# Optimization experiments

Hardware: AMD Instinct MI355X
Metric: run time of the kernel (lower is better)

Reference implementation:

```python
import jax, jax.numpy as jnp
import numpy as np

TOP_K = 2

def setup_inputs() -> dict:
    key = jax.random.key(0)
    k1, k2, k3, k4, k5 = jax.random.split(key, 5)
    B, S, H, E, F = 2, 1024, 1024, 8, 2816
    scale = 0.02
    return {
        "hidden_states": jax.random.normal(k1, (B, S, H), dtype=jnp.float32),
        "gate_w": jax.random.normal(k2, (E, H), dtype=jnp.float32) * scale,
        "w1": jax.random.normal(k3, (E, H, F), dtype=jnp.float32) * scale,
        "w3": jax.random.normal(k4, (E, H, F), dtype=jnp.float32) * scale,
        "w2": jax.random.normal(k5, (E, F, H), dtype=jnp.float32) * scale,
    }

def reference(hidden_states, gate_w, w1, w3, w2):
    B, S, H = hidden_states.shape
    E = gate_w.shape[0]
    x = hidden_states.reshape(-1, H)                      # [T, H]
    T = x.shape[0]
    # Router: logits -> fp32 softmax -> top-k -> renormalize
    router_logits = jnp.einsum('th,eh->te', x, gate_w)    # [T, E]
    probs = jax.nn.softmax(router_logits.astype(jnp.float32), axis=-1)
    top_w, top_i = jax.lax.top_k(probs, TOP_K)            # [T, k]
    top_w = top_w / jnp.sum(top_w, axis=-1, keepdims=True)
    # Scatter normalized top-k weights into dense combine matrix [T, E]
    combine = jnp.zeros((T, E), dtype=probs.dtype)
    combine = combine.at[jnp.arange(T)[:, None], top_i].set(top_w)
    combine = combine.astype(x.dtype)
    # Experts: SwiGLU MLP per expert, weighted combine (dense formulation
    # of gather -> grouped GEMM -> scatter; non-selected experts get weight 0)
    g = jnp.einsum('th,ehf->tef', x, w1)                  # gate proj
    u = jnp.einsum('th,ehf->tef', x, w3)                  # up proj
    act = jax.nn.silu(g) * u                              # [T, E, F]
    act = act * combine[:, :, None]                       # apply routing weight
    out = jnp.einsum('tef,efh->th', act, w2)              # down proj + combine
    final_hidden_states = out.reshape(B, S, H)
    return final_hidden_states, router_logits
```

## Files before the change

### kernel.cpp

```cpp
#include <hip/hip_runtime.h>

typedef unsigned short u16;
typedef unsigned int u32;
typedef __attribute__((ext_vector_type(8))) short bf16x8;
typedef __attribute__((ext_vector_type(4))) float f32x4;

#define T_TOK 2048
#define H_DIM 1024
#define E_NUM 8
#define F_DIM 2816
#define BM 64
#define BN 64
#define BK 32

__device__ __forceinline__ u16 f2bf(float f) {
    u32 b = __float_as_uint(f);
    u32 lsb = (b >> 16) & 1u;
    b += 0x7fffu + lsb;
    return (u16)(b >> 16);
}

__global__ __launch_bounds__(64) void router_kernel(
    const float* __restrict__ x, const float* __restrict__ gw,
    float* __restrict__ logits_out, int* __restrict__ cnt,
    int* __restrict__ tok_list, float* __restrict__ wt_list)
{
    int t = blockIdx.x;
    int lane = threadIdx.x;
    const float* xr = x + (size_t)t * H_DIM;

    float acc[E_NUM];
#pragma unroll
    for (int e = 0; e < E_NUM; e++) acc[e] = 0.f;

    for (int j = 0; j < H_DIM / 64; j++) {
        int idx = j * 64 + lane;
        float xv = xr[idx];
#pragma unroll
        for (int e = 0; e < E_NUM; e++)
            acc[e] += xv * gw[e * H_DIM + idx];
    }
#pragma unroll
    for (int e = 0; e < E_NUM; e++) {
        float v = acc[e];
#pragma unroll
        for (int o = 32; o > 0; o >>= 1) v += __shfl_xor(v, o, 64);
        acc[e] = v;
    }
    if (lane == 0) {
#pragma unroll
        for (int e = 0; e < E_NUM; e++) logits_out[t * E_NUM + e] = acc[e];
        float m = acc[0];
#pragma unroll
        for (int e = 1; e < E_NUM; e++) m = fmaxf(m, acc[e]);
        float p[E_NUM], s = 0.f;
#pragma unroll
        for (int e = 0; e < E_NUM; e++) { p[e] = expf(acc[e] - m); s += p[e]; }
        float inv = 1.f / s;
#pragma unroll
        for (int e = 0; e < E_NUM; e++) p[e] *= inv;
        int i0 = 0;
#pragma unroll
        for (int e = 1; e < E_NUM; e++) if (p[e] > p[i0]) i0 = e;
        int i1 = (i0 == 0) ? 1 : 0;
#pragma unroll
        for (int e = 0; e < E_NUM; e++) if (e != i0 && p[e] > p[i1]) i1 = e;
        float w0 = p[i0], w1 = p[i1];
        float rs = 1.f / (w0 + w1);
        w0 *= rs; w1 *= rs;
        int s0 = atomicAdd(&cnt[i0], 1);
        tok_list[i0 * T_TOK + s0] = t; wt_list[i0 * T_TOK + s0] = w0;
        int s1 = atomicAdd(&cnt[i1], 1);
        tok_list[i1 * T_TOK + s1] = t; wt_list[i1 * T_TOK + s1] = w1;
    }
}

__global__ void offsets_kernel(const int* __restrict__ cnt, int* __restrict__ off)
{
    if (threadIdx.x == 0 && blockIdx.x == 0) {
        int s = 0;
        for (int e = 0; e < E_NUM; e++) {
            off[e] = s;
            s += ((cnt[e] + BM - 1) / BM) * BM;
        }
    }
}

__global__ __launch_bounds__(256) void gemm1_kernel(
    const float* __restrict__ x, const float* __restrict__ w1,
    const float* __restrict__ w3, const int* __restrict__ cnt,
    const int* __restrict__ off, const int* __restrict__ tok_list,
    const float* __restrict__ wt_list, u16* __restrict__ act)
{
    int e = blockIdx.z;
    int m0 = blockIdx.y * BM;
    int n0 = blockIdx.x * BN;
    int c = cnt[e];
    if (m0 >= c) return;

    __shared__ __align__(16) u16 As[BM][40];
    __shared__ __align__(16) u16 B1[BN][40];
    __shared__ __align__(16) u16 B3[BN][40];
    __shared__ int tok_s[BM];
    __shared__ float wt_s[BM];

    int tid = threadIdx.x;
    if (tid < BM) {
        int tok = tok_list[e * T_TOK + m0 + tid];
        tok_s[tid] = tok;
        wt_s[tid] = (tok >= 0) ? wt_list[e * T_TOK + m0 + tid] : 0.f;
    }
    __syncthreads();

    int w = tid >> 6, lane = tid & 63, q = lane >> 4, l15 = lane & 15;
    int wm = (w >> 1) * 32, wn = (w & 1) * 32;

    f32x4 zero = {0.f, 0.f, 0.f, 0.f};
    f32x4 accg[2][2], accu[2][2];
#pragma unroll
    for (int tm = 0; tm < 2; tm++)
#pragma unroll
        for (int tn = 0; tn < 2; tn++) { accg[tm][tn] = zero; accu[tm][tn] = zero; }

    int ar = tid >> 2, ac0 = (tid & 3) * 8;
    int bk = tid >> 3, bf0 = (tid & 7) * 8;
    int tokA = tok_s[ar];
    const size_t wbase = (size_t)e * H_DIM * F_DIM;

    for (int k0 = 0; k0 < H_DIM; k0 += BK) {
        float a8[8];
#pragma unroll
        for (int i = 0; i < 8; i++) a8[i] = 0.f;
        if (tokA >= 0) {
            float4 v0 = *(const float4*)(x + (size_t)tokA * H_DIM + k0 + ac0);
            float4 v1 = *(const float4*)(x + (size_t)tokA * H_DIM + k0 + ac0 + 4);
            a8[0] = v0.x; a8[1] = v0.y; a8[2] = v0.z; a8[3] = v0.w;
            a8[4] = v1.x; a8[5] = v1.y; a8[6] = v1.z; a8[7] = v1.w;
        }
        union { uint4 v; u16 u[8]; } au;
#pragma unroll
        for (int i = 0; i < 8; i++) au.u[i] = f2bf(a8[i]);
        *(uint4*)&As[ar][ac0] = au.v;

        const size_t boff = wbase + (size_t)(k0 + bk) * F_DIM + n0 + bf0;
        float4 b1a = *(const float4*)(w1 + boff);
        float4 b1b = *(const float4*)(w1 + boff + 4);
        float4 b3a = *(const float4*)(w3 + boff);
        float4 b3b = *(const float4*)(w3 + boff + 4);
        float b1v[8] = {b1a.x, b1a.y, b1a.z, b1a.w, b1b.x, b1b.y, b1b.z, b1b.w};
        float b3v[8] = {b3a.x, b3a.y, b3a.z, b3a.w, b3b.x, b3b.y, b3b.z, b3b.w};
#pragma unroll
        for (int i = 0; i < 8; i++) {
            B1[bf0 + i][bk] = f2bf(b1v[i]);
            B3[bf0 + i][bk] = f2bf(b3v[i]);
        }
        __syncthreads();

        bf16x8 a[2], b1f[2], b3f[2];
#pragma unroll
        for (int tm = 0; tm < 2; tm++)
            a[tm] = *(const bf16x8*)&As[wm + tm * 16 + l15][q * 8];
#pragma unroll
        for (int tn = 0; tn < 2; tn++) {
            b1f[tn] = *(const bf16x8*)&B1[wn + tn * 16 + l15][q * 8];
            b3f[tn] = *(const bf16x8*)&B3[wn + tn * 16 + l15][q * 8];
        }
#pragma unroll
        for (int tm = 0; tm < 2; tm++)
#pragma unroll
            for (int tn = 0; tn < 2; tn++) {
                accg[tm][tn] = __builtin_amdgcn_mfma_f32_16x16x32_bf16(a[tm], b1f[tn], accg[tm][tn], 0, 0, 0);
                accu[tm][tn] = __builtin_amdgcn_mfma_f32_16x16x32_bf16(a[tm], b3f[tn], accu[tm][tn], 0, 0, 0);
            }
        __syncthreads();
    }

    int pos0 = off[e] + m0;
#pragma unroll
    for (int tm = 0; tm < 2; tm++)
#pragma unroll
        for (int tn = 0; tn < 2; tn++)
#pragma unroll
            for (int r = 0; r < 4; r++) {
                int row = wm + tm * 16 + q * 4 + r;
                float g = accg[tm][tn][r];
                float u = accu[tm][tn][r];
                float wt = wt_s[row];
                float sg = g / (1.f + expf(-g));
                float val = sg * u * wt;
                int col = n0 + wn + tn * 16 + l15;
                act[(size_t)(pos0 + row) * F_DIM + col] = f2bf(val);
            }
}

__global__ __launch_bounds__(256) void gemm2_kernel(
    const u16* __restrict__ act, const float* __restrict__ w2,
    const int* __restrict__ cnt, const int* __restrict__ off,
    const int* __restrict__ tok_list, float* __restrict__ accum)
{
    int e = blockIdx.z;
    int m0 = blockIdx.y * BM;
    int n0 = blockIdx.x * BN;
    int c = cnt[e];
    if (m0 >= c) return;

    __shared__ __align__(16) u16 As[BM][40];
    __shared__ __align__(16) u16 Bt[BN][40];
    __shared__ int tok_s[BM];

    int tid = threadIdx.x;
    if (tid < BM) tok_s[tid] = tok_list[e * T_TOK + m0 + tid];
    __syncthreads();

    int w = tid >> 6, lane = tid & 63, q = lane >> 4, l15 = lane & 15;
    int wm = (w >> 1) * 32, wn = (w & 1) * 32;

    f32x4 zero = {0.f, 0.f, 0.f, 0.f};
    f32x4 acc[2][2];
#pragma unroll
    for (int tm = 0; tm < 2; tm++)
#pragma unroll
        for (int tn = 0; tn < 2; tn++) acc[tm][tn] = zero;

    int ar = tid >> 2, ac0 = (tid & 3) * 8;
    int bk = tid >> 3, bf0 = (tid & 7) * 8;
    const size_t arow = (size_t)(off[e] + m0 + ar) * F_DIM;
    const size_t wbase = (size_t)e * F_DIM * H_DIM;

    for (int k0 = 0; k0 < F_DIM; k0 += BK) {
        uint4 av = *(const uint4*)(act + arow + k0 + ac0);
        *(uint4*)&As[ar][ac0] = av;

        const size_t boff = wbase + (size_t)(k0 + bk) * H_DIM + n0 + bf0;
        float4 ba = *(const float4*)(w2 + boff);
        float4 bb = *(const float4*)(w2 + boff + 4);
        float bv[8] = {ba.x, ba.y, ba.z, ba.w, bb.x, bb.y, bb.z, bb.w};
#pragma unroll
        for (int i = 0; i < 8; i++) Bt[bf0 + i][bk] = f2bf(bv[i]);
        __syncthreads();

        bf16x8 a[2], b[2];
#pragma unroll
        for (int tm = 0; tm < 2; tm++)
            a[tm] = *(const bf16x8*)&As[wm + tm * 16 + l15][q * 8];
#pragma unroll
        for (int tn = 0; tn < 2; tn++)
            b[tn] = *(const bf16x8*)&Bt[wn + tn * 16 + l15][q * 8];
#pragma unroll
        for (int tm = 0; tm < 2; tm++)
#pragma unroll
            for (int tn = 0; tn < 2; tn++)
                acc[tm][tn] = __builtin_amdgcn_mfma_f32_16x16x32_bf16(a[tm], b[tn], acc[tm][tn], 0, 0, 0);
        __syncthreads();
    }

#pragma unroll
    for (int tm = 0; tm < 2; tm++)
#pragma unroll
        for (int tn = 0; tn < 2; tn++)
#pragma unroll
            for (int r = 0; r < 4; r++) {
                int row = wm + tm * 16 + q * 4 + r;
                int tok = tok_s[row];
                if (tok >= 0) {
                    int col = n0 + wn + tn * 16 + l15;
                    atomicAdd(&accum[(size_t)tok * H_DIM + col], acc[tm][tn][r]);
                }
            }
}

__global__ __launch_bounds__(256) void conv_kernel(
    const float* __restrict__ accum, float* __restrict__ out)
{
    int i = blockIdx.x * 256 + threadIdx.x;
    out[i] = accum[i];
}

extern "C" void kernel_launch(void* const* d_in, const int* in_sizes, int n_in,
                              void* d_out, int out_size, void* d_ws, size_t ws_size,
                              hipStream_t stream) {
    const float* x  = (const float*)d_in[0];
    const float* gw = (const float*)d_in[1];
    const float* w1 = (const float*)d_in[2];
    const float* w3 = (const float*)d_in[3];
    const float* w2 = (const float*)d_in[4];
    float* out = (float*)d_out;

    char* ws = (char*)d_ws;
    int*   cnt      = (int*)(ws);
    int*   off      = (int*)(ws + 64);
    int*   tok_list = (int*)(ws + 128);
    float* wt_list  = (float*)(ws + 128 + 65536);
    float* accum    = (float*)(ws + 128 + 131072);
    u16*   act      = (u16*)(ws + 128 + 131072 + 8388608);

    hipMemsetAsync(cnt, 0, 64, stream);
    hipMemsetAsync(tok_list, 0xFF, 65536, stream);
    hipMemsetAsync(accum, 0, (size_t)T_TOK * H_DIM * 4, stream);

    float* logits_out = out + (size_t)T_TOK * H_DIM;
    router_kernel<<<T_TOK, 64, 0, stream>>>(x, gw, logits_out, cnt, tok_list, wt_list);
    offsets_kernel<<<1, 64, 0, stream>>>(cnt, off);
    gemm1_kernel<<<dim3(F_DIM / BN, T_TOK / BM, E_NUM), 256, 0, stream>>>(
        x, w1, w3, cnt, off, tok_list, wt_list, act);
    gemm2_kernel<<<dim3(H_DIM / BN, T_TOK / BM, E_NUM), 256, 0, stream>>>(
        act, w2, cnt, off, tok_list, accum);
    conv_kernel<<<(T_TOK * H_DIM) / 256, 256, 0, stream>>>(accum, out);
}
```

Measured before the change: 695.7 us.

## Enlarge MoE GEMM tiles, coalesce weight loads, and drop accumulate-copy kernel

Grows the gate/up GEMM tile to 128x128 and the down GEMM tile to 128x64, so each wave computes a 64x64 or 64x32 sub-tile with more MFMAs per shared-memory fetch. Weight tiles are now read with each thread walking down a column, so neighbouring threads read neighbouring addresses, and each thread writes one vectorized shared-memory store instead of eight scalar transposed stores. Global loads are issued before the barrier that guards the shared-memory overwrite, which lets the next tile's loads overlap the current compute and removes the trailing barrier. The down projection now adds atomically straight into the output, so the separate fp32 accumulator and the copy kernel are dropped. The costs are higher register pressure, fewer blocks for small per-expert counts, and more row padding per expert.

New measurement: 667.1 us. 4.1% less time.

```diff
diff --git a/kernel.cpp b/kernel.cpp
--- a/kernel.cpp
+++ b/kernel.cpp
@@ -9,9 +9,11 @@
 #define H_DIM 1024
 #define E_NUM 8
 #define F_DIM 2816
-#define BM 64
-#define BN 64
+#define BM 128
+#define BN1 128
+#define BN2 64
 #define BK 32
+#define LDK 40
 
 __device__ __forceinline__ u16 f2bf(float f) {
     u32 b = __float_as_uint(f);
@@ -86,7 +88,7 @@
     }
 }
 
-__global__ __launch_bounds__(256) void gemm1_kernel(
+__global__ __launch_bounds__(256, 2) void gemm1_kernel(
     const float* __restrict__ x, const float* __restrict__ w1,
     const float* __restrict__ w3, const int* __restrict__ cnt,
     const int* __restrict__ off, const int* __restrict__ tok_list,
@@ -94,13 +96,12 @@
 {
     int e = blockIdx.z;
     int m0 = blockIdx.y * BM;
-    int n0 = blockIdx.x * BN;
-    int c = cnt[e];
-    if (m0 >= c) return;
-
-    __shared__ __align__(16) u16 As[BM][40];
-    __shared__ __align__(16) u16 B1[BN][40];
-    __shared__ __align__(16) u16 B3[BN][40];
+    int n0 = blockIdx.x * BN1;
+    if (m0 >= cnt[e]) return;
+
+    __shared__ __align__(16) u16 As[BM][LDK];
+    __shared__ __align__(16) u16 B1[BN1][LDK];
+    __shared__ __align__(16) u16 B3[BN1][LDK];
     __shared__ int tok_s[BM];
     __shared__ float wt_s[BM];
 
@@ -112,168 +113,179 @@
     }
     __syncthreads();
 
-    int w = tid >> 6, lane = tid & 63, q = lane >> 4, l15 = lane & 15;
-    int wm = (w >> 1) * 32, wn = (w & 1) * 32;
-
-    f32x4 zero = {0.f, 0.f, 0.f, 0.f};
-    f32x4 accg[2][2], accu[2][2];
-#pragma unroll
-    for (int tm = 0; tm < 2; tm++)
-#pragma unroll
-        for (int tn = 0; tn < 2; tn++) { accg[tm][tn] = zero; accu[tm][tn] = zero; }
-
-    int ar = tid >> 2, ac0 = (tid & 3) * 8;
-    int bk = tid >> 3, bf0 = (tid & 7) * 8;
-    int tokA = tok_s[ar];
-    const size_t wbase = (size_t)e * H_DIM * F_DIM;
+    int wid = tid >> 6, lane = tid & 63, q = lane >> 4, l15 = lane & 15;
+    int wr = (wid >> 1) * 64, wc = (wid & 1) * 64;
+
+    const f32x4 zero = {0.f, 0.f, 0.f, 0.f};
+    f32x4 accg[4][4], accu[4][4];
+#pragma unroll
+    for (int i = 0; i < 4; i++)
+#pragma unroll
+        for (int j = 0; j < 4; j++) { accg[i][j] = zero; accu[i][j] = zero; }
+
+    const int arow = tid >> 1, ah = (tid & 1) * 16;
+    const int tokA = tok_s[arow];
+    const int bf = tid & 127, bk0 = (tid >> 7) * 16;
+    const size_t wb = (size_t)e * H_DIM * F_DIM + n0 + bf;
 
     for (int k0 = 0; k0 < H_DIM; k0 += BK) {
-        float a8[8];
-#pragma unroll
-        for (int i = 0; i < 8; i++) a8[i] = 0.f;
+        float a16[16];
         if (tokA >= 0) {
-            float4 v0 = *(const float4*)(x + (size_t)tokA * H_DIM + k0 + ac0);
-            float4 v1 = *(const float4*)(x + (size_t)tokA * H_DIM + k0 + ac0 + 4);
-            a8[0] = v0.x; a8[1] = v0.y; a8[2] = v0.z; a8[3] = v0.w;
-            a8[4] = v1.x; a8[5] = v1.y; a8[6] = v1.z; a8[7] = v1.w;
-        }
-        union { uint4 v; u16 u[8]; } au;
-#pragma unroll
-        for (int i = 0; i < 8; i++) au.u[i] = f2bf(a8[i]);
-        *(uint4*)&As[ar][ac0] = au.v;
-
-        const size_t boff = wbase + (size_t)(k0 + bk) * F_DIM + n0 + bf0;
-        float4 b1a = *(const float4*)(w1 + boff);
-        float4 b1b = *(const float4*)(w1 + boff + 4);
-        float4 b3a = *(const float4*)(w3 + boff);
-        float4 b3b = *(const float4*)(w3 + boff + 4);
-        float b1v[8] = {b1a.x, b1a.y, b1a.z, b1a.w, b1b.x, b1b.y, b1b.z, b1b.w};
-        float b3v[8] = {b3a.x, b3a.y, b3a.z, b3a.w, b3b.x, b3b.y, b3b.z, b3b.w};
-#pragma unroll
-        for (int i = 0; i < 8; i++) {
-            B1[bf0 + i][bk] = f2bf(b1v[i]);
-            B3[bf0 + i][bk] = f2bf(b3v[i]);
+            const float4* xr = (const float4*)(x + (size_t)tokA * H_DIM + k0 + ah);
+            float4 v0 = xr[0], v1 = xr[1], v2 = xr[2], v3 = xr[3];
+            a16[0]=v0.x; a16[1]=v0.y; a16[2]=v0.z;  a16[3]=v0.w;
+            a16[4]=v1.x; a16[5]=v1.y; a16[6]=v1.z;  a16[7]=v1.w;
+            a16[8]=v2.x; a16[9]=v2.y; a16[10]=v2.z; a16[11]=v2.w;
+            a16[12]=v3.x;a16[13]=v3.y;a16[14]=v3.z; a16[15]=v3.w;
+        } else {
+#pragma unroll
+            for (int j = 0; j < 16; j++) a16[j] = 0.f;
+        }
+        float b1v[16], b3v[16];
+        {
+            const size_t base = wb + (size_t)(k0 + bk0) * F_DIM;
+#pragma unroll
+            for (int j = 0; j < 16; j++) {
+                b1v[j] = w1[base + (size_t)j * F_DIM];
+                b3v[j] = w3[base + (size_t)j * F_DIM];
+            }
         }
         __syncthreads();
-
-        bf16x8 a[2], b1f[2], b3f[2];
-#pragma unroll
-        for (int tm = 0; tm < 2; tm++)
-            a[tm] = *(const bf16x8*)&As[wm + tm * 16 + l15][q * 8];
-#pragma unroll
-        for (int tn = 0; tn < 2; tn++) {
-            b1f[tn] = *(const bf16x8*)&B1[wn + tn * 16 + l15][q * 8];
-            b3f[tn] = *(const bf16x8*)&B3[wn + tn * 16 + l15][q * 8];
-        }
-#pragma unroll
-        for (int tm = 0; tm < 2; tm++)
-#pragma unroll
-            for (int tn = 0; tn < 2; tn++) {
-                accg[tm][tn] = __builtin_amdgcn_mfma_f32_16x16x32_bf16(a[tm], b1f[tn], accg[tm][tn], 0, 0, 0);
-                accu[tm][tn] = __builtin_amdgcn_mfma_f32_16x16x32_bf16(a[tm], b3f[tn], accu[tm][tn], 0, 0, 0);
+        {
+            union { uint4 v[2]; u16 u[16]; } pu;
+#pragma unroll
+            for (int j = 0; j < 16; j++) pu.u[j] = f2bf(a16[j]);
+            *(uint4*)&As[arow][ah]     = pu.v[0];
+            *(uint4*)&As[arow][ah + 8] = pu.v[1];
+#pragma unroll
+            for (int j = 0; j < 16; j++) pu.u[j] = f2bf(b1v[j]);
+            *(uint4*)&B1[bf][bk0]     = pu.v[0];
+            *(uint4*)&B1[bf][bk0 + 8] = pu.v[1];
+#pragma unroll
+            for (int j = 0; j < 16; j++) pu.u[j] = f2bf(b3v[j]);
+            *(uint4*)&B3[bf][bk0]     = pu.v[0];
+            *(uint4*)&B3[bf][bk0 + 8] = pu.v[1];
+        }
+        __syncthreads();
+
+        bf16x8 a[4], f1[4], f3[4];
+#pragma unroll
+        for (int tm = 0; tm < 4; tm++)
+            a[tm] = *(const bf16x8*)&As[wr + tm * 16 + l15][q * 8];
+#pragma unroll
+        for (int tn = 0; tn < 4; tn++) {
+            f1[tn] = *(const bf16x8*)&B1[wc + tn * 16 + l15][q * 8];
+            f3[tn] = *(const bf16x8*)&B3[wc + tn * 16 + l15][q * 8];
+        }
+#pragma unroll
+        for (int tm = 0; tm < 4; tm++)
+#pragma unroll
+            for (int tn = 0; tn < 4; tn++) {
+                accg[tm][tn] = __builtin_amdgcn_mfma_f32_16x16x32_bf16(a[tm], f1[tn], accg[tm][tn], 0, 0, 0);
+                accu[tm][tn] = __builtin_amdgcn_mfma_f32_16x16x32_bf16(a[tm], f3[tn], accu[tm][tn], 0, 0, 0);
             }
-        __syncthreads();
-    }
-
-    int pos0 = off[e] + m0;
-#pragma unroll
-    for (int tm = 0; tm < 2; tm++)
-#pragma unroll
-        for (int tn = 0; tn < 2; tn++)
-#pragma unroll
-            for (int r = 0; r < 4; r++) {
-                int row = wm + tm * 16 + q * 4 + r;
+    }
+
+    const int pos0 = off[e] + m0;
+#pragma unroll
+    for (int tm = 0; tm < 4; tm++) {
+        const int row = wr + tm * 16 + q * 4;
+#pragma unroll
+        for (int r = 0; r < 4; r++) {
+            const float wt = wt_s[row + r];
+            u16* aptr = act + (size_t)(pos0 + row + r) * F_DIM + n0 + wc + l15;
+#pragma unroll
+            for (int tn = 0; tn < 4; tn++) {
                 float g = accg[tm][tn][r];
                 float u = accu[tm][tn][r];
-                float wt = wt_s[row];
                 float sg = g / (1.f + expf(-g));
-                float val = sg * u * wt;
-                int col = n0 + wn + tn * 16 + l15;
-                act[(size_t)(pos0 + row) * F_DIM + col] = f2bf(val);
+                aptr[tn * 16] = f2bf(sg * u * wt);
             }
-}
-
-__global__ __launch_bounds__(256) void gemm2_kernel(
+        }
+    }
+}
+
+__global__ __launch_bounds__(256, 3) void gemm2_kernel(
     const u16* __restrict__ act, const float* __restrict__ w2,
     const int* __restrict__ cnt, const int* __restrict__ off,
-    const int* __restrict__ tok_list, float* __restrict__ accum)
+    const int* __restrict__ tok_list, float* __restrict__ out)
 {
     int e = blockIdx.z;
     int m0 = blockIdx.y * BM;
-    int n0 = blockIdx.x * BN;
-    int c = cnt[e];
-    if (m0 >= c) return;
-
-    __shared__ __align__(16) u16 As[BM][40];
-    __shared__ __align__(16) u16 Bt[BN][40];
+    int n0 = blockIdx.x * BN2;
+    if (m0 >= cnt[e]) return;
+
+    __shared__ __align__(16) u16 As[BM][LDK];
+    __shared__ __align__(16) u16 Bt[BN2][LDK];
     __shared__ int tok_s[BM];
 
     int tid = threadIdx.x;
     if (tid < BM) tok_s[tid] = tok_list[e * T_TOK + m0 + tid];
     __syncthreads();
 
-    int w = tid >> 6, lane = tid & 63, q = lane >> 4, l15 = lane & 15;
-    int wm = (w >> 1) * 32, wn = (w & 1) * 32;
-
-    f32x4 zero = {0.f, 0.f, 0.f, 0.f};
-    f32x4 acc[2][2];
-#pragma unroll
-    for (int tm = 0; tm < 2; tm++)
-#pragma unroll
-        for (int tn = 0; tn < 2; tn++) acc[tm][tn] = zero;
-
-    int ar = tid >> 2, ac0 = (tid & 3) * 8;
-    int bk = tid >> 3, bf0 = (tid & 7) * 8;
-    const size_t arow = (size_t)(off[e] + m0 + ar) * F_DIM;
-    const size_t wbase = (size_t)e * F_DIM * H_DIM;
+    int wid = tid >> 6, lane = tid & 63, q = lane >> 4, l15 = lane & 15;
+    int wr = (wid >> 1) * 64, wc = (wid & 1) * 32;
+
+    const f32x4 zero = {0.f, 0.f, 0.f, 0.f};
+    f32x4 acc[4][2];
+#pragma unroll
+    for (int i = 0; i < 4; i++)
+#pragma unroll
+        for (int j = 0; j < 2; j++) acc[i][j] = zero;
+
+    const int arow = tid >> 1, ah = (tid & 1) * 16;
+    const size_t abase = (size_t)(off[e] + m0 + arow) * F_DIM + ah;
+    const int bh = tid & 63, bk0 = (tid >> 6) * 8;
+    const size_t wb = (size_t)e * F_DIM * H_DIM + n0 + bh;
 
     for (int k0 = 0; k0 < F_DIM; k0 += BK) {
-        uint4 av = *(const uint4*)(act + arow + k0 + ac0);
-        *(uint4*)&As[ar][ac0] = av;
-
-        const size_t boff = wbase + (size_t)(k0 + bk) * H_DIM + n0 + bf0;
-        float4 ba = *(const float4*)(w2 + boff);
-        float4 bb = *(const float4*)(w2 + boff + 4);
-        float bv[8] = {ba.x, ba.y, ba.z, ba.w, bb.x, bb.y, bb.z, bb.w};
-#pragma unroll
-        for (int i = 0; i < 8; i++) Bt[bf0 + i][bk] = f2bf(bv[i]);
+        uint4 av0 = *(const uint4*)(act + abase + k0);
+        uint4 av1 = *(const uint4*)(act + abase + k0 + 8);
+        float bv[8];
+        {
+            const size_t base = wb + (size_t)(k0 + bk0) * H_DIM;
+#pragma unroll
+            for (int j = 0; j < 8; j++) bv[j] = w2[base + (size_t)j * H_DIM];
+        }
         __syncthreads();
-
-        bf16x8 a[2], b[2];
-#pragma unroll
-        for (int tm = 0; tm < 2; tm++)
-            a[tm] = *(const bf16x8*)&As[wm + tm * 16 + l15][q * 8];
+        *(uint4*)&As[arow][ah]     = av0;
+        *(uint4*)&As[arow][ah + 8] = av1;
+        {
+            union { uint4 v; u16 u[8]; } pu;
+#pragma unroll
+            for (int j = 0; j < 8; j++) pu.u[j] = f2bf(bv[j]);
+            *(uint4*)&Bt[bh][bk0] = pu.v;
+        }
+        __syncthreads();
+
+        bf16x8 a[4], b[2];
+#pragma unroll
+        for (int tm = 0; tm < 4; tm++)
+            a[tm] = *(const bf16x8*)&As[wr + tm * 16 + l15][q * 8];
 #pragma unroll
         for (int tn = 0; tn < 2; tn++)
-            b[tn] = *(const bf16x8*)&Bt[wn + tn * 16 + l15][q * 8];
-#pragma unroll
-        for (int tm = 0; tm < 2; tm++)
+            b[tn] = *(const bf16x8*)&Bt[wc + tn * 16 + l15][q * 8];
+#pragma unroll
+        for (int tm = 0; tm < 4; tm++)
 #pragma unroll
             for (int tn = 0; tn < 2; tn++)
                 acc[tm][tn] = __builtin_amdgcn_mfma_f32_16x16x32_bf16(a[tm], b[tn], acc[tm][tn], 0, 0, 0);
-        __syncthreads();
-    }
-
-#pragma unroll
-    for (int tm = 0; tm < 2; tm++)
-#pragma unroll
-        for (int tn = 0; tn < 2; tn++)
-#pragma unroll
-            for (int r = 0; r < 4; r++) {
-                int row = wm + tm * 16 + q * 4 + r;
-                int tok = tok_s[row];
-                if (tok >= 0) {
-                    int col = n0 + wn + tn * 16 + l15;
-                    atomicAdd(&accum[(size_t)tok * H_DIM + col], acc[tm][tn][r]);
-                }
+    }
+
+#pragma unroll
+    for (int tm = 0; tm < 4; tm++) {
+        const int row = wr + tm * 16 + q * 4;
+#pragma unroll
+        for (int r = 0; r < 4; r++) {
+            const int tok = tok_s[row + r];
+            if (tok >= 0) {
+                float* optr = out + (size_t)tok * H_DIM + n0 + wc + l15;
+#pragma unroll
+                for (int tn = 0; tn < 2; tn++)
+                    atomicAdd(&optr[tn * 16], acc[tm][tn][r]);
             }
-}
-
-__global__ __launch_bounds__(256) void conv_kernel(
-    const float* __restrict__ accum, float* __restrict__ out)
-{
-    int i = blockIdx.x * 256 + threadIdx.x;
-    out[i] = accum[i];
+        }
+    }
 }
 
 extern "C" void kernel_launch(void* const* d_in, const int* in_sizes, int n_in,
@@ -291,19 +303,17 @@
     int*   off      = (int*)(ws + 64);
     int*   tok_list = (int*)(ws + 128);
     float* wt_list  = (float*)(ws + 128 + 65536);
-    float* accum    = (float*)(ws + 128 + 131072);
-    u16*   act      = (u16*)(ws + 128 + 131072 + 8388608);
+    u16*   act      = (u16*)(ws + 128 + 131072);
 
     hipMemsetAsync(cnt, 0, 64, stream);
     hipMemsetAsync(tok_list, 0xFF, 65536, stream);
-    hipMemsetAsync(accum, 0, (size_t)T_TOK * H_DIM * 4, stream);
+    hipMemsetAsync(out, 0, (size_t)T_TOK * H_DIM * sizeof(float), stream);
 
     float* logits_out = out + (size_t)T_TOK * H_DIM;
     router_kernel<<<T_TOK, 64, 0, stream>>>(x, gw, logits_out, cnt, tok_list, wt_list);
     offsets_kernel<<<1, 64, 0, stream>>>(cnt, off);
-    gemm1_kernel<<<dim3(F_DIM / BN, T_TOK / BM, E_NUM), 256, 0, stream>>>(
+    gemm1_kernel<<<dim3(F_DIM / BN1, T_TOK / BM, E_NUM), 256, 0, stream>>>(
         x, w1, w3, cnt, off, tok_list, wt_list, act);
-    gemm2_kernel<<<dim3(H_DIM / BN, T_TOK / BM, E_NUM), 256, 0, stream>>>(
-        act, w2, cnt, off, tok_list, accum);
-    conv_kernel<<<(T_TOK * H_DIM) / 256, 256, 0, stream>>>(accum, out);
-}
+    gemm2_kernel<<<dim3(H_DIM / BN2, T_TOK / BM, E_NUM), 256, 0, stream>>>(
+        act, w2, cnt, off, tok_list, out);
+}
```
